# Optimization experiments

Hardware: AMD Instinct MI355X
Metric: run time of the kernel (lower is better)

## Reference

```python
import jax, jax.numpy as jnp
import numpy as np

IN_CAPS, IN_DIM, OUT_CAPS, OUT_DIM = 2048, 8, 32, 16
NUM_ROUTING = 3
EPS = 1e-9


def squash(s):
    # s: [..., out_dim]
    s2 = jnp.sum(s * s, axis=-1, keepdims=True)
    return (s2 / (1.0 + s2)) * (s / jnp.sqrt(s2 + EPS))


def setup_inputs() -> dict:
    key = jax.random.key(0)
    kx, kw = jax.random.split(key)
    x = jax.random.normal(kx, (64, IN_CAPS, IN_DIM), dtype=jnp.float32)
    W = jax.random.normal(kw, (1, IN_CAPS, OUT_CAPS, OUT_DIM, IN_DIM), dtype=jnp.float32) * 0.01
    return {"x": x, "W": W}


def reference(x, W):
    # u_hat[b,i,o,j] = sum_d W[0,i,o,j,d] * x[b,i,d]
    u_hat = jnp.einsum('iojd,bid->bioj', W[0], x)  # [B, in_caps, out_caps, out_dim]
    b_ij = jnp.zeros(u_hat.shape[:3], dtype=u_hat.dtype)  # [B, in_caps, out_caps]
    v_j = None
    for r in range(NUM_ROUTING):
        c_ij = jax.nn.softmax(b_ij, axis=2)[..., None]  # [B, in, out, 1]
        s_j = jnp.sum(c_ij * u_hat, axis=1)             # [B, out, out_dim]
        v_j = squash(s_j)
        if r < NUM_ROUTING - 1:
            b_ij = b_ij + jnp.einsum('bioj,boj->bio', u_hat, v_j)
    return v_j
```

## Files before the change

### kernel.cpp

```cpp
#include <hip/hip_runtime.h>
#include <math.h>


#define IC 2048
#define OC 32
#define OD 16
#define B_N 64
#define S_ELEMS (B_N * OC * OD)
#define IPB 8
#define ISTR (IC / IPB)
#define BPB 32
#define BG  (B_N / BPB)
#define NB  8

typedef float nt4 __attribute__((ext_vector_type(4)));

template <int CTRL>
__device__ __forceinline__ float dpp_add(float v) {
    int r = __builtin_amdgcn_update_dpp(0, __float_as_int(v), CTRL, 0xf, 0xf, true);
    return v + __int_as_float(r);
}


template <int FIRST>
__launch_bounds__(256, 1)
__global__ void caps_pass(const float* __restrict__ Wg,
                          const float* __restrict__ xg,
                          const float* __restrict__ vs,
                          float* __restrict__ part)
{
    __shared__ float4 WS[2][16 * 65];
    __shared__ float4 XS[2][64];
    float* accred = (float*)WS;

    const int tid  = threadIdx.x;
    const int lane = tid & 63;
    const int w    = tid >> 6;
    const int o    = lane & 31;
    const int jh   = lane >> 5;
    const int c    = (o << 1) | jh;

    const int is   = blockIdx.x & (ISTR - 1);
    const int bg   = blockIdx.x >> 8;
    const int bblk = bg * BPB;
    const int bq   = bblk + w * NB;

    const float4* wq = (const float4*)Wg;
    const float4* xq = (const float4*)xg;

    float4 va[NB], vb[NB];
    if (!FIRST) {
#pragma unroll
        for (int n = 0; n < NB; ++n) {
            const float4* vp = (const float4*)(vs + (size_t)(bq + n) * 512 + o * 16 + jh * 8);
            va[n] = vp[0];
            vb[n] = vp[1];
        }
    }

    float acc[NB][8];
#pragma unroll
    for (int n = 0; n < NB; ++n)
#pragma unroll
        for (int jj = 0; jj < 8; ++jj) acc[n][jj] = 0.0f;

    {
        const size_t base = (size_t)(is * IPB) * 1024;
#pragma unroll
        for (int q = 0; q < 4; ++q) {
            const int G = q * 256 + tid;
            const float4 val = wq[base + G];
            const int oo = G >> 5, j = (G >> 1) & 15, dh = G & 1;
            WS[0][((dh << 3) | (j & 7)) * 65 + ((oo << 1) | (j >> 3))] = val;
        }
        if (tid < 64)
            XS[0][tid] = xq[((size_t)(bblk + (tid >> 1)) * IC + is * IPB) * 2 + (tid & 1)];
    }

    for (int il = 0; il < IPB; ++il) {
        const int p = il & 1;
        __syncthreads();

        float4 g0 = {}, g1 = {}, g2 = {}, g3 = {}, gx = {};
        const bool more = (il + 1 < IPB);
        if (more) {
            const size_t base = (size_t)(is * IPB + il + 1) * 1024;
            g0 = wq[base + 0 * 256 + tid];
            g1 = wq[base + 1 * 256 + tid];
            g2 = wq[base + 2 * 256 + tid];
            g3 = wq[base + 3 * 256 + tid];
            if (tid < 64)
                gx = xq[((size_t)(bblk + (tid >> 1)) * IC + is * IPB + il + 1) * 2 + (tid & 1)];
        }

        float4 fr0[8], fr1[8];
#pragma unroll
        for (int jj = 0; jj < 8; ++jj) {
            fr0[jj] = WS[p][jj * 65 + c];
            fr1[jj] = WS[p][(8 + jj) * 65 + c];
        }

#pragma unroll
        for (int n = 0; n < NB; ++n) {
            const float4 xa = XS[p][(w * NB + n) * 2];
            const float4 xb = XS[p][(w * NB + n) * 2 + 1];

            float u[8];
#pragma unroll
            for (int jj = 0; jj < 8; ++jj) {
                float t = fr0[jj].x * xa.x;
                t = fmaf(fr0[jj].y, xa.y, t);
                t = fmaf(fr0[jj].z, xa.z, t);
                t = fmaf(fr0[jj].w, xa.w, t);
                t = fmaf(fr1[jj].x, xb.x, t);
                t = fmaf(fr1[jj].y, xb.y, t);
                t = fmaf(fr1[jj].z, xb.z, t);
                t = fmaf(fr1[jj].w, xb.w, t);
                u[jj] = t;
            }

            float cc;
            if (FIRST) {
                cc = 1.0f;
            } else {
                float bp = u[0] * va[n].x;
                bp = fmaf(u[1], va[n].y, bp);
                bp = fmaf(u[2], va[n].z, bp);
                bp = fmaf(u[3], va[n].w, bp);
                bp = fmaf(u[4], vb[n].x, bp);
                bp = fmaf(u[5], vb[n].y, bp);
                bp = fmaf(u[6], vb[n].z, bp);
                bp = fmaf(u[7], vb[n].w, bp);
                bp += __shfl_xor(bp, 32);
                const float e = __expf(bp);
                float se = e;
                se = dpp_add<0x128>(se);
                se = dpp_add<0x124>(se);
                se = dpp_add<0x122>(se);
                se = dpp_add<0x121>(se);
                se += __shfl_xor(se, 16);
                cc = e * __builtin_amdgcn_rcpf(se);
            }
#pragma unroll
            for (int jj = 0; jj < 8; ++jj)
                acc[n][jj] = fmaf(cc, u[jj], acc[n][jj]);
        }

        if (more) {
            auto put = [&](int G, float4 val) {
                const int oo = G >> 5, j = (G >> 1) & 15, dh = G & 1;
                WS[p ^ 1][((dh << 3) | (j & 7)) * 65 + ((oo << 1) | (j >> 3))] = val;
            };
            put(0 * 256 + tid, g0);
            put(1 * 256 + tid, g1);
            put(2 * 256 + tid, g2);
            put(3 * 256 + tid, g3);
            if (tid < 64) XS[p ^ 1][tid] = gx;
        }
    }

    const float scale = FIRST ? (1.0f / 32.0f) : 1.0f;
#pragma unroll
    for (int t = 0; t < 2; ++t) {
        __syncthreads();
        if ((w >> 1) == t) {
            const int bl0 = (w & 1) * NB;
#pragma unroll
            for (int n = 0; n < NB; ++n)
#pragma unroll
                for (int jj = 0; jj < 8; ++jj)
                    accred[(bl0 + n) * 520 + jj * 64 + c] = acc[n][jj] * scale;
        }
        __syncthreads();
        float* dstbase = part + (size_t)is * S_ELEMS + (size_t)(bblk + t * 16) * 512;
#pragma unroll
        for (int k = 0; k < 8; ++k) {
            const int q  = k * 256 + tid;
            const int e0 = q * 4;
            const int bl = e0 >> 9;
            const int oo = (e0 >> 4) & 31;
            const int j0 = e0 & 15;
            nt4 v;
            v.x = accred[bl * 520 + ((j0 + 0) & 7) * 64 + ((oo << 1) | ((j0 + 0) >> 3))];
            v.y = accred[bl * 520 + ((j0 + 1) & 7) * 64 + ((oo << 1) | ((j0 + 1) >> 3))];
            v.z = accred[bl * 520 + ((j0 + 2) & 7) * 64 + ((oo << 1) | ((j0 + 2) >> 3))];
            v.w = accred[bl * 520 + ((j0 + 3) & 7) * 64 + ((oo << 1) | ((j0 + 3) >> 3))];
            __builtin_nontemporal_store(v, (nt4*)(dstbase + e0));
        }
    }
}

template <int MODE>
__global__ void caps_reduce(const float* __restrict__ part,
                            float* __restrict__ vsum,
                            float* __restrict__ out)
{
    __shared__ float red[256];
    const int tid = threadIdx.x;
    const int e   = blockIdx.x * 64 + (tid & 63);
    const int ks  = tid >> 6;
    float s = 0.0f;
#pragma unroll 8
    for (int m = 0; m < 64; ++m)
        s += __builtin_nontemporal_load(part + (size_t)(ks * 64 + m) * S_ELEMS + e);
    red[tid] = s;
    __syncthreads();
    if (tid < 64) {
        s = red[tid] + red[tid + 64] + red[tid + 128] + red[tid + 192];
        float s2 = s * s;
        s2 += __shfl_xor(s2, 1);
        s2 += __shfl_xor(s2, 2);
        s2 += __shfl_xor(s2, 4);
        s2 += __shfl_xor(s2, 8);
        const float v = s * (s2 / ((1.0f + s2) * sqrtf(s2 + 1e-9f)));
        if (MODE == 2)      out[e] = v;
        else if (MODE == 0) vsum[e] = v;
        else                vsum[e] += v;
    }
}

extern "C" void kernel_launch(void* const* d_in, const int* in_sizes, int n_in,
                              void* d_out, int out_size, void* d_ws, size_t ws_size,
                              hipStream_t stream)
{
    const float* x = (const float*)d_in[0];
    const float* W = (const float*)d_in[1];
    float* out = (float*)d_out;

    float* part = (float*)d_ws;
    float* vsum = part + (size_t)ISTR * S_ELEMS;

    const dim3 g(BG * ISTR);
    const dim3 b(256);
    const dim3 rg(S_ELEMS / 64);

    caps_pass<1><<<g, b, 0, stream>>>(W, x, nullptr, part);
    caps_reduce<0><<<rg, b, 0, stream>>>(part, vsum, out);
    caps_pass<0><<<g, b, 0, stream>>>(W, x, vsum, part);
    caps_reduce<1><<<rg, b, 0, stream>>>(part, vsum, out);
    caps_pass<0><<<g, b, 0, stream>>>(W, x, vsum, part);
    caps_reduce<2><<<rg, b, 0, stream>>>(part, vsum, out);
}
```

Before: 197.0 us.

## Store routing partial sums in fp16 and double in-capsule split count

Partial sums written by each routing pass are now stored as fp16 instead of fp32, halving the bytes of the partial buffer. The in-capsule chunk per block is halved, so twice as many blocks run, and all x rows for the chunk are loaded up front instead of double-buffered. The reduce kernel reads half2 pairs, processes two elements per thread, and sums 128 partials per thread slice. The aim is to cut partial-buffer memory traffic and raise parallelism, at the cost of fp16 rounding in the partials and twice as many partial slices to reduce.

```diff
diff --git a/kernel.cpp b/kernel.cpp
--- a/kernel.cpp
+++ b/kernel.cpp
@@ -1,4 +1,5 @@
 #include <hip/hip_runtime.h>
+#include <hip/hip_fp16.h>
 #include <math.h>
 
 
@@ -7,13 +8,13 @@
 #define OD 16
 #define B_N 64
 #define S_ELEMS (B_N * OC * OD)
-#define IPB 8
+#define IPB 4
 #define ISTR (IC / IPB)
 #define BPB 32
 #define BG  (B_N / BPB)
 #define NB  8
 
-typedef float nt4 __attribute__((ext_vector_type(4)));
+typedef unsigned short us8 __attribute__((ext_vector_type(8)));
 
 template <int CTRL>
 __device__ __forceinline__ float dpp_add(float v) {
@@ -27,10 +28,10 @@
 __global__ void caps_pass(const float* __restrict__ Wg,
                           const float* __restrict__ xg,
                           const float* __restrict__ vs,
-                          float* __restrict__ part)
+                          __half* __restrict__ part)
 {
     __shared__ float4 WS[2][16 * 65];
-    __shared__ float4 XS[2][64];
+    __shared__ float4 XS[IPB][64];
     float* accred = (float*)WS;
 
     const int tid  = threadIdx.x;
@@ -41,12 +42,13 @@
     const int c    = (o << 1) | jh;
 
     const int is   = blockIdx.x & (ISTR - 1);
-    const int bg   = blockIdx.x >> 8;
+    const int bg   = blockIdx.x >> 9;
     const int bblk = bg * BPB;
     const int bq   = bblk + w * NB;
 
     const float4* wq = (const float4*)Wg;
     const float4* xq = (const float4*)xg;
+    const int i0 = is * IPB;
 
     float4 va[NB], vb[NB];
     if (!FIRST) {
@@ -65,7 +67,7 @@
         for (int jj = 0; jj < 8; ++jj) acc[n][jj] = 0.0f;
 
     {
-        const size_t base = (size_t)(is * IPB) * 1024;
+        const size_t base = (size_t)i0 * 1024;
 #pragma unroll
         for (int q = 0; q < 4; ++q) {
             const int G = q * 256 + tid;
@@ -73,24 +75,24 @@
             const int oo = G >> 5, j = (G >> 1) & 15, dh = G & 1;
             WS[0][((dh << 3) | (j & 7)) * 65 + ((oo << 1) | (j >> 3))] = val;
         }
-        if (tid < 64)
-            XS[0][tid] = xq[((size_t)(bblk + (tid >> 1)) * IC + is * IPB) * 2 + (tid & 1)];
+        {
+            const int bl = tid >> 3, il = (tid >> 1) & 3, hf = tid & 1;
+            XS[il][bl * 2 + hf] = xq[((size_t)(bblk + bl) * IC + i0 + il) * 2 + hf];
+        }
     }
 
     for (int il = 0; il < IPB; ++il) {
         const int p = il & 1;
         __syncthreads();
 
-        float4 g0 = {}, g1 = {}, g2 = {}, g3 = {}, gx = {};
+        float4 g0 = {}, g1 = {}, g2 = {}, g3 = {};
         const bool more = (il + 1 < IPB);
         if (more) {
-            const size_t base = (size_t)(is * IPB + il + 1) * 1024;
+            const size_t base = (size_t)(i0 + il + 1) * 1024;
             g0 = wq[base + 0 * 256 + tid];
             g1 = wq[base + 1 * 256 + tid];
             g2 = wq[base + 2 * 256 + tid];
             g3 = wq[base + 3 * 256 + tid];
-            if (tid < 64)
-                gx = xq[((size_t)(bblk + (tid >> 1)) * IC + is * IPB + il + 1) * 2 + (tid & 1)];
         }
 
         float4 fr0[8], fr1[8];
@@ -102,8 +104,8 @@
 
 #pragma unroll
         for (int n = 0; n < NB; ++n) {
-            const float4 xa = XS[p][(w * NB + n) * 2];
-            const float4 xb = XS[p][(w * NB + n) * 2 + 1];
+            const float4 xa = XS[il][(w * NB + n) * 2];
+            const float4 xb = XS[il][(w * NB + n) * 2 + 1];
 
             float u[8];
 #pragma unroll
@@ -155,7 +157,6 @@
             put(1 * 256 + tid, g1);
             put(2 * 256 + tid, g2);
             put(3 * 256 + tid, g3);
-            if (tid < 64) XS[p ^ 1][tid] = gx;
         }
     }
 
@@ -172,50 +173,69 @@
                     accred[(bl0 + n) * 520 + jj * 64 + c] = acc[n][jj] * scale;
         }
         __syncthreads();
-        float* dstbase = part + (size_t)is * S_ELEMS + (size_t)(bblk + t * 16) * 512;
-#pragma unroll
-        for (int k = 0; k < 8; ++k) {
-            const int q  = k * 256 + tid;
-            const int e0 = q * 4;
-            const int bl = e0 >> 9;
-            const int oo = (e0 >> 4) & 31;
-            const int j0 = e0 & 15;
-            nt4 v;
-            v.x = accred[bl * 520 + ((j0 + 0) & 7) * 64 + ((oo << 1) | ((j0 + 0) >> 3))];
-            v.y = accred[bl * 520 + ((j0 + 1) & 7) * 64 + ((oo << 1) | ((j0 + 1) >> 3))];
-            v.z = accred[bl * 520 + ((j0 + 2) & 7) * 64 + ((oo << 1) | ((j0 + 2) >> 3))];
-            v.w = accred[bl * 520 + ((j0 + 3) & 7) * 64 + ((oo << 1) | ((j0 + 3) >> 3))];
-            __builtin_nontemporal_store(v, (nt4*)(dstbase + e0));
+        __half* dstbase = part + (size_t)is * S_ELEMS + (size_t)(bblk + t * 16) * 512;
+#pragma unroll
+        for (int k2 = 0; k2 < 4; ++k2) {
+            const int q   = k2 * 256 + tid;
+            const int bl  = q >> 6;
+            const int oo  = (q >> 1) & 31;
+            const int j0h = q & 1;
+            const int cb  = (oo << 1) | j0h;
+            const float* src = accred + bl * 520 + cb;
+            us8 hv;
+#pragma unroll
+            for (int k = 0; k < 8; ++k)
+                hv[k] = __half_as_ushort(__float2half(src[k * 64]));
+            __builtin_nontemporal_store(hv, (us8*)(dstbase + q * 8));
         }
     }
 }
 
 template <int MODE>
-__global__ void caps_reduce(const float* __restrict__ part,
+__global__ void caps_reduce(const __half* __restrict__ part,
                             float* __restrict__ vsum,
                             float* __restrict__ out)
 {
-    __shared__ float red[256];
-    const int tid = threadIdx.x;
-    const int e   = blockIdx.x * 64 + (tid & 63);
-    const int ks  = tid >> 6;
-    float s = 0.0f;
+    __shared__ float2 red[4][64];
+    const int tid  = threadIdx.x;
+    const int lane = tid & 63;
+    const int ks   = tid >> 6;
+    const int e2   = blockIdx.x * 64 + lane;
+    const unsigned* p32 = (const unsigned*)part;
+
+    float sx = 0.0f, sy = 0.0f;
 #pragma unroll 8
-    for (int m = 0; m < 64; ++m)
-        s += __builtin_nontemporal_load(part + (size_t)(ks * 64 + m) * S_ELEMS + e);
-    red[tid] = s;
+    for (int m = 0; m < 128; ++m) {
+        const unsigned u =
+            __builtin_nontemporal_load(p32 + (size_t)(ks * 128 + m) * (S_ELEMS / 2) + e2);
+        const __half2 h = __builtin_bit_cast(__half2, u);
+        const float2 f = __half22float2(h);
+        sx += f.x;
+        sy += f.y;
+    }
+    red[ks][lane] = make_float2(sx, sy);
     __syncthreads();
     if (tid < 64) {
-        s = red[tid] + red[tid + 64] + red[tid + 128] + red[tid + 192];
-        float s2 = s * s;
+        float2 a = red[0][lane], b2 = red[1][lane], c2 = red[2][lane], d2 = red[3][lane];
+        const float ex = a.x + b2.x + c2.x + d2.x;
+        const float ey = a.y + b2.y + c2.y + d2.y;
+        float s2 = ex * ex + ey * ey;
         s2 += __shfl_xor(s2, 1);
         s2 += __shfl_xor(s2, 2);
         s2 += __shfl_xor(s2, 4);
-        s2 += __shfl_xor(s2, 8);
-        const float v = s * (s2 / ((1.0f + s2) * sqrtf(s2 + 1e-9f)));
-        if (MODE == 2)      out[e] = v;
-        else if (MODE == 0) vsum[e] = v;
-        else                vsum[e] += v;
+        const float m = s2 / ((1.0f + s2) * sqrtf(s2 + 1e-9f));
+        const float vx = ex * m, vy = ey * m;
+        if (MODE == 2) {
+            ((float2*)out)[e2] = make_float2(vx, vy);
+        } else {
+            float2 nv;
+            if (MODE == 0) nv = make_float2(vx, vy);
+            else {
+                float2 old = ((float2*)vsum)[e2];
+                nv = make_float2(old.x + vx, old.y + vy);
+            }
+            ((float2*)vsum)[e2] = nv;
+        }
     }
 }
 
@@ -227,12 +247,12 @@
     const float* W = (const float*)d_in[1];
     float* out = (float*)d_out;
 
-    float* part = (float*)d_ws;
-    float* vsum = part + (size_t)ISTR * S_ELEMS;
+    __half* part = (__half*)d_ws;
+    float*  vsum = (float*)(part + (size_t)ISTR * S_ELEMS);
 
     const dim3 g(BG * ISTR);
     const dim3 b(256);
-    const dim3 rg(S_ELEMS / 64);
+    const dim3 rg(S_ELEMS / 128);
 
     caps_pass<1><<<g, b, 0, stream>>>(W, x, nullptr, part);
     caps_reduce<0><<<rg, b, 0, stream>>>(part, vsum, out);
```

Result: slower. 217.7 us (+10.5%).
